# Kernel tuning notes

Measured on AMD Instinct MI355X. Metric: run time of the kernel, lower is better.

Reference implementation:

```python
import jax, jax.numpy as jnp
import numpy as np

B, S, D, E, K = 4, 4096, 2048, 64, 2


def setup_inputs() -> dict:
    key = jax.random.key(0)
    k1, k2, k3 = jax.random.split(key, 3)
    x = jax.random.normal(k1, (B, S, D), dtype=jnp.float32)
    W = jax.random.normal(k2, (D, E), dtype=jnp.float32) / np.sqrt(D)
    b = jnp.zeros((E,), dtype=jnp.float32)
    noise = jax.random.normal(k3, (B, S, E), dtype=jnp.float32)
    return {"x": x, "W": W, "b": b, "noise": noise}


def reference(x, W, b, noise):
    # logits = Linear(x); noisy gating adds N(0,1)/10 noise
    logits = jnp.einsum('bsd,de->bse', x, W) + b  # [B,S,E]
    logits = logits + noise * 0.1
    scores = jax.nn.softmax(logits, axis=-1)      # [B,S,E]
    topk_scores, topk_indices = jax.lax.top_k(scores, K)  # [B,S,K]
    return topk_scores, topk_indices, scores
```

## Files before the change

kernel.cpp:

```cpp
#include <hip/hip_runtime.h>
#include <math.h>

#define BS_TOT 16384
#define DDIM   2048
#define NEXP   64
#define TOPK   2

#define NW     16
#define RPB    64
#define DSLICE (DDIM / NW)
#define TK     8
#define NTILE  (DSLICE / TK)

__global__ __launch_bounds__(1024)
void router_kernel(const float* __restrict__ x, const float* __restrict__ W,
                   const float* __restrict__ bias, const float* __restrict__ noise,
                   float* __restrict__ out)
{
    __shared__ float smem[NW][2][TK][NEXP];
    float (*lacc)[NEXP + 1] = (float (*)[NEXP + 1])smem;

    const int tid  = threadIdx.x;
    const int lane = tid & 63;
    const int wv   = __builtin_amdgcn_readfirstlane(tid >> 6);
    const int row0 = blockIdx.x * RPB;
    const int rg   = lane >> 3;
    const int er   = lane & 7;

    float acc[8][8];
#pragma unroll
    for (int i = 0; i < 8; ++i)
#pragma unroll
        for (int j = 0; j < 8; ++j) acc[i][j] = 0.0f;

    const int dw0 = wv * DSLICE;
    const float* xg = x + (size_t)(row0 + lane) * DDIM + dw0;
    const int    wk = lane >> 3;
    const int    we = (lane & 7) * 8;
    const float* wg = W + (size_t)(dw0 + wk) * NEXP + we;

    float4 gx0 = *(const float4*)(xg);
    float4 gx1 = *(const float4*)(xg + 4);
    float4 gw0 = *(const float4*)(wg);
    float4 gw1 = *(const float4*)(wg + 4);

#pragma unroll 1
    for (int t = 0; t < NTILE; ++t) {
        smem[wv][0][0][lane] = gx0.x;
        smem[wv][0][1][lane] = gx0.y;
        smem[wv][0][2][lane] = gx0.z;
        smem[wv][0][3][lane] = gx0.w;
        smem[wv][0][4][lane] = gx1.x;
        smem[wv][0][5][lane] = gx1.y;
        smem[wv][0][6][lane] = gx1.z;
        smem[wv][0][7][lane] = gx1.w;
        *(float4*)&smem[wv][1][wk][we]     = gw0;
        *(float4*)&smem[wv][1][wk][we + 4] = gw1;

        if (t + 1 < NTILE) {
            const float* xn = xg + (t + 1) * TK;
            gx0 = *(const float4*)(xn);
            gx1 = *(const float4*)(xn + 4);
            const float* wn = wg + (size_t)(t + 1) * TK * NEXP;
            gw0 = *(const float4*)(wn);
            gw1 = *(const float4*)(wn + 4);
        }

#pragma unroll 1
        for (int k = 0; k < TK; ++k) {
            const float4 a0 = *(const float4*)&smem[wv][0][k][rg * 8];
            const float4 a1 = *(const float4*)&smem[wv][0][k][rg * 8 + 4];
            const float4 b0 = *(const float4*)&smem[wv][1][k][er * 8];
            const float4 b1 = *(const float4*)&smem[wv][1][k][er * 8 + 4];
            const float av[8] = {a0.x, a0.y, a0.z, a0.w, a1.x, a1.y, a1.z, a1.w};
            const float bv[8] = {b0.x, b0.y, b0.z, b0.w, b1.x, b1.y, b1.z, b1.w};
#pragma unroll
            for (int i = 0; i < 8; ++i)
#pragma unroll
                for (int j = 0; j < 8; ++j)
                    acc[i][j] = fmaf(av[i], bv[j], acc[i][j]);
        }
    }

    __syncthreads();
    for (int i = tid; i < RPB * (NEXP + 1); i += 1024) ((float*)lacc)[i] = 0.0f;
    __syncthreads();
#pragma unroll
    for (int i = 0; i < 8; ++i)
#pragma unroll
        for (int j = 0; j < 8; ++j)
            atomicAdd(&lacc[rg * 8 + i][er * 8 + j], acc[i][j]);
    __syncthreads();

    const float blane = bias[lane];
    float* const scores_out = out + 2 * BS_TOT * TOPK;
    float* const iout       = out + BS_TOT * TOPK;

#pragma unroll
    for (int j = 0; j < RPB / NW; ++j) {
        const int rl  = wv * (RPB / NW) + j;
        const int r2  = row0 + rl;
        const float v = lacc[rl][lane] + blane + 0.1f * noise[(size_t)r2 * NEXP + lane];

        float m = v;
#pragma unroll
        for (int off = 1; off < 64; off <<= 1) m = fmaxf(m, __shfl_xor(m, off));
        const float p = __expf(v - m);
        float s = p;
#pragma unroll
        for (int off = 1; off < 64; off <<= 1) s += __shfl_xor(s, off);
        const float sc = p * (1.0f / s);

        scores_out[(size_t)r2 * NEXP + lane] = sc;

        float a1 = v, a2 = -INFINITY;
        int   i1 = lane, i2 = 0x7fffffff;
#pragma unroll
        for (int off = 1; off < 64; off <<= 1) {
            const float o1 = __shfl_xor(a1, off), o2 = __shfl_xor(a2, off);
            const int  oi1 = __shfl_xor(i1, off), oi2 = __shfl_xor(i2, off);
            if (o1 > a1 || (o1 == a1 && oi1 < i1)) {
                if (a1 > o2 || (a1 == o2 && i1 < oi2)) { a2 = a1; i2 = i1; }
                else                                   { a2 = o2; i2 = oi2; }
                a1 = o1; i1 = oi1;
            } else {
                if (o1 > a2 || (o1 == a2 && oi1 < i2)) { a2 = o1; i2 = oi1; }
            }
        }
        const float s1 = __shfl(sc, i1);
        const float s2 = __shfl(sc, i2);
        if (lane == 0) {
            out[(size_t)r2 * TOPK + 0]  = s1;
            out[(size_t)r2 * TOPK + 1]  = s2;
            iout[(size_t)r2 * TOPK + 0] = (float)i1;
            iout[(size_t)r2 * TOPK + 1] = (float)i2;
        }
    }
}

extern "C" void kernel_launch(void* const* d_in, const int* in_sizes, int n_in,
                              void* d_out, int out_size, void* d_ws, size_t ws_size,
                              hipStream_t stream)
{
    const float* x     = (const float*)d_in[0];
    const float* W     = (const float*)d_in[1];
    const float* bias  = (const float*)d_in[2];
    const float* noise = (const float*)d_in[3];
    float* out = (float*)d_out;
    (void)in_sizes; (void)n_in; (void)out_size; (void)d_ws; (void)ws_size;

    hipLaunchKernelGGL(router_kernel, dim3(BS_TOT / RPB), dim3(1024), 0, stream,
                       x, W, bias, noise, out);
}
```

Before: 312.1 us.

## Load W tiles directly into LDS and double K-tile depth

W tiles are now fetched with global_load_lds (direct global-to-LDS) instead of going through registers. The K tile grows from 8 to 16 and the inner k loop is partially unrolled. Explicit s_waitcnt calls order the LDS writes and the async loads. The aim is to cut register staging and the per-tile overhead of the loop. The cost is that correctness now depends on the hand-coded waitcnt encodings and on LDS aliasing within each wave. The next W tile is only issued after compute finishes, so its latency is not fully hidden.

```diff
diff --git a/kernel.cpp b/kernel.cpp
--- a/kernel.cpp
+++ b/kernel.cpp
@@ -9,15 +9,22 @@
 #define NW     16
 #define RPB    64
 #define DSLICE (DDIM / NW)
-#define TK     8
+#define TK     16
 #define NTILE  (DSLICE / TK)
+
+
+__device__ __forceinline__ void gload_lds16(const float* g, float* l) {
+    __builtin_amdgcn_global_load_lds(
+        (const __attribute__((address_space(1))) unsigned int*)(g),
+        (__attribute__((address_space(3))) unsigned int*)(l), 16, 0, 0);
+}
 
 __global__ __launch_bounds__(1024)
 void router_kernel(const float* __restrict__ x, const float* __restrict__ W,
                    const float* __restrict__ bias, const float* __restrict__ noise,
                    float* __restrict__ out)
 {
-    __shared__ float smem[NW][2][TK][NEXP];
+    __shared__ float smem[NW][2048];
     float (*lacc)[NEXP + 1] = (float (*)[NEXP + 1])smem;
 
     const int tid  = threadIdx.x;
@@ -27,6 +34,9 @@
     const int rg   = lane >> 3;
     const int er   = lane & 7;
 
+    float* const xt = &smem[wv][0];
+    float* const wt = &smem[wv][1024];
+
     float acc[8][8];
 #pragma unroll
     for (int i = 0; i < 8; ++i)
@@ -35,43 +45,38 @@
 
     const int dw0 = wv * DSLICE;
     const float* xg = x + (size_t)(row0 + lane) * DDIM + dw0;
-    const int    wk = lane >> 3;
-    const int    we = (lane & 7) * 8;
-    const float* wg = W + (size_t)(dw0 + wk) * NEXP + we;
+    const int wkk = lane >> 4;
+    const int wcc = (lane & 15) * 4;
 
-    float4 gx0 = *(const float4*)(xg);
-    float4 gx1 = *(const float4*)(xg + 4);
-    float4 gw0 = *(const float4*)(wg);
-    float4 gw1 = *(const float4*)(wg + 4);
+    float4 gx[4];
+#pragma unroll
+    for (int q = 0; q < 4; ++q) gx[q] = *(const float4*)(xg + q * 4);
+#pragma unroll
+    for (int i = 0; i < 4; ++i)
+        gload_lds16(W + (size_t)(dw0 + 4 * i + wkk) * NEXP + wcc, wt + i * 256);
 
 #pragma unroll 1
     for (int t = 0; t < NTILE; ++t) {
-        smem[wv][0][0][lane] = gx0.x;
-        smem[wv][0][1][lane] = gx0.y;
-        smem[wv][0][2][lane] = gx0.z;
-        smem[wv][0][3][lane] = gx0.w;
-        smem[wv][0][4][lane] = gx1.x;
-        smem[wv][0][5][lane] = gx1.y;
-        smem[wv][0][6][lane] = gx1.z;
-        smem[wv][0][7][lane] = gx1.w;
-        *(float4*)&smem[wv][1][wk][we]     = gw0;
-        *(float4*)&smem[wv][1][wk][we + 4] = gw1;
-
+#pragma unroll
+        for (int q = 0; q < 4; ++q) {
+            xt[(q * 4 + 0) * 64 + lane] = gx[q].x;
+            xt[(q * 4 + 1) * 64 + lane] = gx[q].y;
+            xt[(q * 4 + 2) * 64 + lane] = gx[q].z;
+            xt[(q * 4 + 3) * 64 + lane] = gx[q].w;
+        }
+        __builtin_amdgcn_s_waitcnt(0x0F70);
         if (t + 1 < NTILE) {
             const float* xn = xg + (t + 1) * TK;
-            gx0 = *(const float4*)(xn);
-            gx1 = *(const float4*)(xn + 4);
-            const float* wn = wg + (size_t)(t + 1) * TK * NEXP;
-            gw0 = *(const float4*)(wn);
-            gw1 = *(const float4*)(wn + 4);
+#pragma unroll
+            for (int q = 0; q < 4; ++q) gx[q] = *(const float4*)(xn + q * 4);
         }
 
-#pragma unroll 1
+#pragma unroll 4
         for (int k = 0; k < TK; ++k) {
-            const float4 a0 = *(const float4*)&smem[wv][0][k][rg * 8];
-            const float4 a1 = *(const float4*)&smem[wv][0][k][rg * 8 + 4];
-            const float4 b0 = *(const float4*)&smem[wv][1][k][er * 8];
-            const float4 b1 = *(const float4*)&smem[wv][1][k][er * 8 + 4];
+            const float4 a0 = *(const float4*)&xt[k * 64 + rg * 8];
+            const float4 a1 = *(const float4*)&xt[k * 64 + rg * 8 + 4];
+            const float4 b0 = *(const float4*)&wt[k * 64 + er * 8];
+            const float4 b1 = *(const float4*)&wt[k * 64 + er * 8 + 4];
             const float av[8] = {a0.x, a0.y, a0.z, a0.w, a1.x, a1.y, a1.z, a1.w};
             const float bv[8] = {b0.x, b0.y, b0.z, b0.w, b1.x, b1.y, b1.z, b1.w};
 #pragma unroll
@@ -79,6 +84,14 @@
 #pragma unroll
                 for (int j = 0; j < 8; ++j)
                     acc[i][j] = fmaf(av[i], bv[j], acc[i][j]);
+        }
+
+        __builtin_amdgcn_s_waitcnt(0xC07F);
+        if (t + 1 < NTILE) {
+            const float* wn = W + (size_t)(dw0 + (t + 1) * TK) * NEXP;
+#pragma unroll
+            for (int i = 0; i < 4; ++i)
+                gload_lds16(wn + (size_t)(4 * i + wkk) * NEXP + wcc, wt + i * 256);
         }
     }
 
```

Result: faster. 305.6 us (-2.1%).
